# Kernel tuning notes

Hardware: AMD Instinct MI355X
Metric: run time of the kernel (lower is better)

## Reference

```python
import jax, jax.numpy as jnp
import numpy as np

EPS = 1e-8
LN_EPS = 1e-5

def _ln(x, g, b):
    m = x.mean(-1, keepdims=True)
    v = ((x - m) ** 2).mean(-1, keepdims=True)
    return (x - m) * jax.lax.rsqrt(v + LN_EPS) * g + b

def _rbf(d, n_rbf):
    # standard protein RBF embedding: gaussians on [0, 20] Angstrom
    mu = jnp.linspace(0.0, 20.0, n_rbf)
    sigma = 20.0 / n_rbf
    return jnp.exp(-(((d[..., None] - mu) / sigma) ** 2))

def setup_inputs() -> dict:
    N, K, CS, CZ, G, RBF = 1024, 16, 256, 128, 16, 64
    key = jax.random.key(0)
    ks = jax.random.split(key, 24)
    s = 0.02
    inp = {
        'node_features': jax.random.normal(ks[0], (N, CS), jnp.float32),
        'trans': jax.random.normal(ks[1], (N, 3), jnp.float32) * 10.0,
        'src_edge_features': jax.random.normal(ks[2], (N, K, CZ), jnp.float32),
        'dst_edge_features': jax.random.normal(ks[3], (N, K, CZ), jnp.float32),
        # params
        'ln_src_g': jnp.ones((CZ,)), 'ln_src_b': jnp.zeros((CZ,)),
        'ln_dst_g': jnp.ones((CZ,)), 'ln_dst_b': jnp.zeros((CZ,)),
        'W_nl': jax.random.normal(ks[4], (G, CS)) * s, 'b_nl': jnp.zeros((G,)),
        'W_nr': jax.random.normal(ks[5], (G, CS)) * s, 'b_nr': jnp.zeros((G,)),
        'W_ep': jax.random.normal(ks[6], (CZ, CZ)) * s, 'b_ep': jnp.zeros((CZ,)),
        'W_eg': jax.random.normal(ks[7], (CZ, CZ)) * s, 'b_eg': jnp.zeros((CZ,)),
        'W_dg': jax.random.normal(ks[8], (CZ, G, G)) * s, 'b_dg': jnp.zeros((CZ,)),
        'W_dp': jax.random.normal(ks[9], (CZ, RBF)) * s, 'b_dp': jnp.zeros((CZ,)),
        'ln_out_g': jnp.ones((CZ,)), 'ln_out_b': jnp.zeros((CZ,)),
        'W_lo': jax.random.normal(ks[10], (CZ, CZ)) * s, 'b_lo': jnp.zeros((CZ,)),
        'W_og': jax.random.normal(ks[11], (CZ, CZ)) * s, 'b_og': jnp.zeros((CZ,)),
        # int / mask args (KNN form)
        'src_edge_index': jax.random.randint(ks[12], (2, N, K), 0, N, jnp.int32),
        'dst_edge_index': jax.random.randint(ks[13], (2, N, K), 0, N, jnp.int32),
        'src_mask': jnp.ones((N, K), bool),
        'dst_mask': jnp.ones((N, K), bool),
    }
    return inp

def reference(node_features, trans, src_edge_features, dst_edge_features,
              ln_src_g, ln_src_b, ln_dst_g, ln_dst_b,
              W_nl, b_nl, W_nr, b_nr, W_ep, b_ep, W_eg, b_eg,
              W_dg, b_dg, W_dp, b_dp, ln_out_g, ln_out_b,
              W_lo, b_lo, W_og, b_og,
              src_edge_index, dst_edge_index, src_mask, dst_mask):
    N, K, CZ = src_edge_features.shape
    src_ln = _ln(src_edge_features, ln_src_g, ln_src_b)   # [N,K,CZ]
    dst_ln = _ln(dst_edge_features, ln_dst_g, ln_dst_b)
    node_left = node_features @ W_nl.T + b_nl              # [N,G]
    node_right = node_features @ W_nr.T + b_nr
    e1 = node_left[src_edge_index[0]]                      # [N,K,G]
    e2 = node_right[dst_edge_index[0]]                     # [N,K,G]
    # triangle gate: fuse outer product [N,K,K,G,G] with dist_gate Linear
    t = jnp.einsum('nia,zab->nizb', e1, W_dg)
    gate3 = jnp.einsum('nizb,njb->nijz', t, e2) + b_dg     # [N,K,K,CZ]
    t1 = trans[src_edge_index[0]]                          # [N,K,3]
    t2 = trans[dst_edge_index[0]]
    d = jnp.linalg.norm(t1[:, :, None, :] - t2[:, None, :, :] + EPS, axis=-1)  # [N,K,K]
    distf = _rbf(d, W_dp.shape[1]) @ W_dp.T + b_dp         # [N,K,K,CZ]
    mask3 = (src_mask[:, :, None] & dst_mask[:, None, :])[..., None]
    edge3 = jax.nn.sigmoid(gate3) * distf * mask3          # [N,K,K,CZ]
    edge2 = jax.nn.sigmoid(src_ln @ W_eg.T + b_eg) * (src_ln @ W_ep.T + b_ep)  # [N,K,CZ]
    # batched per-channel combine: sum over dst slot j
    upd = jnp.einsum('nijz,njz->niz', edge3, edge2)        # [N,K,CZ]
    upd = _ln(upd, ln_out_g, ln_out_b) @ W_lo.T + b_lo
    upd = upd * jax.nn.sigmoid(dst_ln @ W_og.T + b_og)
    upd = upd * dst_mask[..., None]                        # knn -> sparse (masked flatten)
    return upd.reshape(N * K, CZ)
```

## Files before the change

### kernel.cpp

```cpp
#include <hip/hip_runtime.h>
#include <hip/hip_bf16.h>
#include <stdint.h>

#define N_    1024
#define K_    16
#define CZ_   128
#define G_    16
#define RBF_  64
#define CS_   256

typedef const float* fp;
typedef _Float16 f16x8 __attribute__((ext_vector_type(8)));
typedef _Float16 h2    __attribute__((ext_vector_type(2)));
typedef float f32x4    __attribute__((ext_vector_type(4)));

#define MFMA16(A,B,C) __builtin_amdgcn_mfma_f32_16x16x32_f16(A,B,C,0,0,0)

#define OFF_EGH 0
#define OFF_EPH 16384
#define OFF_EPL 32768
#define OFF_OGH 49152
#define OFF_LOH 65536
#define OFF_LOL 81920
#define OFF_DPH 98304
#define OFF_NLH 106496
#define OFF_NRH 110592
#define OFF_DGT 114688

__device__ __forceinline__ float sigm(float x){ return 1.0f/(1.0f+__expf(-x)); }
__device__ __forceinline__ unsigned short f2h(float v){
  union{_Float16 h; unsigned short u;} c; c.h = (_Float16)v; return c.u;
}
__device__ __forceinline__ float h2f(unsigned short u){
  union{unsigned short u; _Float16 h;} c; c.u = u; return (float)c.h;
}
__device__ __forceinline__ unsigned int pk2(float a, float b){
  union{h2 h; unsigned int u;} c; c.h[0] = (_Float16)a; c.h[1] = (_Float16)b; return c.u;
}
__device__ __forceinline__ f16x8 ldh8(const unsigned short* p){
  union{uint4 u; f16x8 h;} c; c.u = *(const uint4*)p; return c.h;
}

__global__ __launch_bounds__(256) void repack(
    fp W_eg, fp W_ep, fp W_og, fp W_lo, fp W_dp, fp W_nl, fp W_nr, fp W_dg,
    unsigned short* __restrict__ ws)
{
  int t = blockIdx.x*256 + threadIdx.x;
  int stride = gridDim.x*256;
  for (int i = t; i < 16384; i += stride) {
    ws[OFF_EGH+i] = f2h(W_eg[i]);
    ws[OFF_OGH+i] = f2h(W_og[i]);
    float e = W_ep[i]; _Float16 h = (_Float16)e;
    union{_Float16 hh; unsigned short u;} c1; c1.hh = h;
    ws[OFF_EPH+i] = c1.u;
    ws[OFF_EPL+i] = f2h(e - (float)h);
    float l = W_lo[i]; _Float16 hl = (_Float16)l;
    union{_Float16 hh; unsigned short u;} c2; c2.hh = hl;
    ws[OFF_LOH+i] = c2.u;
    ws[OFF_LOL+i] = f2h(l - (float)hl);
  }
  for (int i = t; i < 8192; i += stride)
    ws[OFF_DPH+i] = f2h(W_dp[i]);
  for (int i = t; i < 4096; i += stride) {
    ws[OFF_NLH+i] = f2h(W_nl[i]);
    ws[OFF_NRH+i] = f2h(W_nr[i]);
  }
  for (int i = t; i < 32768; i += stride) {
    int z = i >> 8, rem = i & 255, b = rem >> 4, a = rem & 15;
    ws[OFF_DGT+i] = f2h(W_dg[z*256 + a*16 + b]);
  }
}

__global__ __launch_bounds__(512, 4) void tri_fused3(
    fp nf, fp trans, fp srcef, fp dstef,
    fp ln_src_g, fp ln_src_b, fp ln_dst_g, fp ln_dst_b,
    fp b_nl, fp b_nr, fp b_eg, fp b_ep, fp b_og,
    fp b_dg, fp b_dp, fp ln_out_g, fp ln_out_b, fp b_lo,
    const int* __restrict__ sidx, const int* __restrict__ didx,
    const unsigned short* __restrict__ ws,
    float* __restrict__ out)
{
  __shared__ __align__(16) unsigned short bufA[8448];
  __shared__ __align__(16) unsigned short bufB[6528];
  __shared__ __align__(16) unsigned short rbfH[16*64*16];
  __shared__ __align__(16) unsigned short edge2h[128*18];
  __shared__ __align__(16) unsigned short sogh[16*128];
  __shared__ __align__(16) unsigned short e1h[16*16];
  __shared__ __align__(16) unsigned short e2h[16*18];
  __shared__ __align__(16) float t1f[16][4];
  __shared__ __align__(16) float t2f[16][4];

  unsigned short* nflh = bufA;
  float* updf = (float*)bufA;
  unsigned short* srcH = bufB;
  unsigned short* srcL = bufB + 2176;
  unsigned short* dstH = bufB + 4352;
  unsigned short* updH = bufB;
  unsigned short* updL = bufB + 2176;

  const int n   = blockIdx.x;
  const int tid = threadIdx.x;
  const int wv  = tid >> 6;
  const int lnn = tid & 63;
  const int lm  = lnn & 15;
  const int lq  = lnn >> 4;

  {
    int row = tid >> 4;
    int c0  = (tid & 15) * 16;
    int r16 = row & 15;
    int idx = (row < 16) ? sidx[n*K_ + r16] : didx[n*K_ + r16];
    const float* src = nf + idx*CS_ + c0;
    float4 a = *(const float4*)(src);
    float4 b = *(const float4*)(src+4);
    float4 c = *(const float4*)(src+8);
    float4 d = *(const float4*)(src+12);
    uint4 u0, u1;
    u0.x = pk2(a.x,a.y); u0.y = pk2(a.z,a.w); u0.z = pk2(b.x,b.y); u0.w = pk2(b.z,b.w);
    u1.x = pk2(c.x,c.y); u1.y = pk2(c.z,c.w); u1.z = pk2(d.x,d.y); u1.w = pk2(d.z,d.w);
    *(uint4*)&nflh[row*264 + c0]     = u0;
    *(uint4*)&nflh[row*264 + c0 + 8] = u1;
    if (tid < 32) {
      int k = tid & 15;
      int id2 = (tid < 16) ? sidx[n*K_ + k] : didx[n*K_ + k];
      float* tf = (tid < 16) ? &t1f[k][0] : &t2f[k][0];
      tf[0] = trans[id2*3+0]; tf[1] = trans[id2*3+1]; tf[2] = trans[id2*3+2];
    }
  }
  {
    int row = tid >> 4;
    int c0  = (tid & 15) * 8;
    int r16 = row & 15;
    bool isSrc = row < 16;
    const float* base = (isSrc ? srcef : dstef) + (n*K_ + r16)*CZ_ + c0;
    float4 xa = *(const float4*)base;
    float4 xb = *(const float4*)(base+4);
    float x[8] = {xa.x,xa.y,xa.z,xa.w,xb.x,xb.y,xb.z,xb.w};
    float s = x[0]+x[1]+x[2]+x[3]+x[4]+x[5]+x[6]+x[7];
    s += __shfl_xor(s,1); s += __shfl_xor(s,2);
    s += __shfl_xor(s,4); s += __shfl_xor(s,8);
    float m = s * 0.0078125f;
    float q = 0.f;
    #pragma unroll
    for (int i = 0; i < 8; ++i) { float d = x[i]-m; q += d*d; }
    q += __shfl_xor(q,1); q += __shfl_xor(q,2);
    q += __shfl_xor(q,4); q += __shfl_xor(q,8);
    float rv = rsqrtf(q * 0.0078125f + 1e-5f);
    fp gp = isSrc ? ln_src_g : ln_dst_g;
    fp bp = isSrc ? ln_src_b : ln_dst_b;
    float y[8];
    #pragma unroll
    for (int i = 0; i < 8; ++i) y[i] = (x[i]-m)*rv*gp[c0+i] + bp[c0+i];
    if (isSrc) {
      float l[8];
      #pragma unroll
      for (int i = 0; i < 8; ++i) { _Float16 h0 = (_Float16)y[i]; l[i] = y[i] - (float)h0; }
      uint4 uh, ul;
      uh.x = pk2(y[0],y[1]); uh.y = pk2(y[2],y[3]); uh.z = pk2(y[4],y[5]); uh.w = pk2(y[6],y[7]);
      ul.x = pk2(l[0],l[1]); ul.y = pk2(l[2],l[3]); ul.z = pk2(l[4],l[5]); ul.w = pk2(l[6],l[7]);
      *(uint4*)&srcH[r16*136 + c0] = uh;
      *(uint4*)&srcL[r16*136 + c0] = ul;
    } else {
      uint4 uh;
      uh.x = pk2(y[0],y[1]); uh.y = pk2(y[2],y[3]); uh.z = pk2(y[4],y[5]); uh.w = pk2(y[6],y[7]);
      *(uint4*)&dstH[r16*136 + c0] = uh;
    }
  }
  __syncthreads();

  if (wv < 2) {
    const unsigned short* Wh = ws + (wv ? OFF_NRH : OFF_NLH);
    fp bb = wv ? b_nr : b_nl;
    const unsigned short* arow = nflh + (wv*16 + lm)*264;
    f32x4 acc = {0.f,0.f,0.f,0.f};
    #pragma unroll
    for (int kb = 0; kb < 256; kb += 32) {
      f16x8 ah = ldh8(arow + kb + lq*8);
      f16x8 bh = ldh8(Wh + lm*256 + kb + lq*8);
      acc = MFMA16(ah, bh, acc);
    }
    float bias = bb[lm];
    #pragma unroll
    for (int r = 0; r < 4; ++r) {
      if (wv) e2h[(lq*4+r)*18 + lm] = f2h(acc[r] + bias);
      else    e1h[(lq*4+r)*16 + lm] = f2h(acc[r] + bias);
    }
  }

  {
    const int z = wv*16 + lm;
    f32x4 aeg = {0.f,0.f,0.f,0.f}, aep = {0.f,0.f,0.f,0.f}, aog = {0.f,0.f,0.f,0.f};
    #pragma unroll
    for (int kb = 0; kb < 128; kb += 32) {
      f16x8 sh = ldh8(srcH + lm*136 + kb + lq*8);
      f16x8 sl = ldh8(srcL + lm*136 + kb + lq*8);
      f16x8 dh = ldh8(dstH + lm*136 + kb + lq*8);
      f16x8 wegv = ldh8(ws + OFF_EGH + z*128 + kb + lq*8);
      f16x8 weph = ldh8(ws + OFF_EPH + z*128 + kb + lq*8);
      f16x8 wepl = ldh8(ws + OFF_EPL + z*128 + kb + lq*8);
      f16x8 wogv = ldh8(ws + OFF_OGH + z*128 + kb + lq*8);
      aeg = MFMA16(sh, wegv, aeg);
      aep = MFMA16(sh, weph, aep);
      aep = MFMA16(sl, weph, aep);
      aep = MFMA16(sh, wepl, aep);
      aog = MFMA16(dh, wogv, aog);
    }
    float beg = b_eg[z], bep = b_ep[z], bog = b_og[z];
    #pragma unroll
    for (int r = 0; r < 4; ++r) {
      int j = lq*4 + r;
      edge2h[z*18 + j] = f2h(sigm(aeg[r]+beg) * (aep[r]+bep));
      sogh[j*128 + z]  = f2h(sigm(aog[r]+bog));
    }
  }

  {
    const float inv_sigma = 3.2f;
    const float mustep = 20.0f/63.0f;
    #pragma unroll
    for (int i2 = 0; i2 < 2; ++i2) {
      int i = wv*2 + i2;
      float dx = t1f[i][0]-t2f[lm][0]+1e-8f;
      float dy = t1f[i][1]-t2f[lm][1]+1e-8f;
      float dz = t1f[i][2]-t2f[lm][2]+1e-8f;
      float d = sqrtf(dx*dx+dy*dy+dz*dz);
      #pragma unroll
      for (int kh = 0; kh < 2; ++kh) {
        union { f16x8 h; uint4 u; } cv;
        #pragma unroll
        for (int c = 0; c < 8; ++c) {
          int k = kh*32 + lq*8 + c;
          float t = (d - (float)k*mustep) * inv_sigma;
          cv.h[c] = (_Float16)__expf(-t*t);
        }
        *(uint4*)&rbfH[(i*64+lnn)*16 + kh*8] = cv.u;
      }
    }
  }
  __syncthreads();

  {
    const int z = wv*16 + lm;
    f16x8 Bdg[8];
    #pragma unroll
    for (int q = 0; q < 8; ++q)
      Bdg[q] = ldh8(ws + OFF_DGT + z*256 + q*32 + lq*8);
    f16x8 Bdp0 = ldh8(ws + OFF_DPH + z*64 + lq*8);
    f16x8 Bdp1 = ldh8(ws + OFF_DPH + z*64 + 32 + lq*8);
    const float bdg = b_dg[z], bdp = b_dp[z];
    _Float16 e2s[8];
    #pragma unroll
    for (int q = 0; q < 8; ++q) {
      union{unsigned short u; _Float16 h;} c;
      c.u = e2h[lm*18 + 2*q + (lq>>1)];
      e2s[q] = c.h;
    }
    for (int i = 0; i < 16; ++i) {
      f16x8 e1v = ldh8(e1h + i*16 + (lq&1)*8);
      f32x4 accg = {0.f,0.f,0.f,0.f};
      #pragma unroll
      for (int q = 0; q < 8; ++q) {
        f16x8 av;
        _Float16 sc = e2s[q];
        #pragma unroll
        for (int c = 0; c < 8; ++c) av[c] = e1v[c] * sc;
        accg = MFMA16(av, Bdg[q], accg);
      }
      f16x8 r0 = ldh8(&rbfH[(i*64+lnn)*16]);
      f16x8 r1 = ldh8(&rbfH[(i*64+lnn)*16 + 8]);
      f32x4 accp = {0.f,0.f,0.f,0.f};
      accp = MFMA16(r0, Bdp0, accp);
      accp = MFMA16(r1, Bdp1, accp);
      float s = 0.f;
      #pragma unroll
      for (int r = 0; r < 4; ++r) {
        int j = lq*4 + r;
        float e2v = h2f(edge2h[z*18 + j]);
        s += sigm(accg[r]+bdg) * (accp[r]+bdp) * e2v;
      }
      s += __shfl_xor(s,16); s += __shfl_xor(s,32);
      if (lq == 0) updf[i*132 + z] = s;
    }
  }
  __syncthreads();

  {
    int row = tid >> 5;
    int c0  = (tid & 31) * 4;
    float4 x = *(const float4*)&updf[row*132 + c0];
    float s = x.x+x.y+x.z+x.w;
    s += __shfl_xor(s,1,32); s += __shfl_xor(s,2,32); s += __shfl_xor(s,4,32);
    s += __shfl_xor(s,8,32); s += __shfl_xor(s,16,32);
    float m = s * 0.0078125f;
    float q = (x.x-m)*(x.x-m)+(x.y-m)*(x.y-m)+(x.z-m)*(x.z-m)+(x.w-m)*(x.w-m);
    q += __shfl_xor(q,1,32); q += __shfl_xor(q,2,32); q += __shfl_xor(q,4,32);
    q += __shfl_xor(q,8,32); q += __shfl_xor(q,16,32);
    float rv = rsqrtf(q*0.0078125f + 1e-5f);
    float y0 = (x.x-m)*rv*ln_out_g[c0+0] + ln_out_b[c0+0];
    float y1 = (x.y-m)*rv*ln_out_g[c0+1] + ln_out_b[c0+1];
    float y2 = (x.z-m)*rv*ln_out_g[c0+2] + ln_out_b[c0+2];
    float y3 = (x.w-m)*rv*ln_out_g[c0+3] + ln_out_b[c0+3];
    _Float16 h0 = (_Float16)y0, h1 = (_Float16)y1, h2v = (_Float16)y2, h3 = (_Float16)y3;
    uint2 uh, ul;
    uh.x = pk2(y0,y1); uh.y = pk2(y2,y3);
    ul.x = pk2(y0-(float)h0, y1-(float)h1);
    ul.y = pk2(y2-(float)h2v, y3-(float)h3);
    __syncthreads();
    *(uint2*)&updH[row*136 + c0] = uh;
    *(uint2*)&updL[row*136 + c0] = ul;
  }
  __syncthreads();

  {
    const int z = wv*16 + lm;
    f32x4 acc = {0.f,0.f,0.f,0.f};
    #pragma unroll
    for (int kb = 0; kb < 128; kb += 32) {
      f16x8 ah = ldh8(updH + lm*136 + kb + lq*8);
      f16x8 al = ldh8(updL + lm*136 + kb + lq*8);
      f16x8 bh = ldh8(ws + OFF_LOH + z*128 + kb + lq*8);
      f16x8 bl = ldh8(ws + OFF_LOL + z*128 + kb + lq*8);
      acc = MFMA16(ah, bh, acc);
      acc = MFMA16(al, bh, acc);
      acc = MFMA16(ah, bl, acc);
    }
    float blo = b_lo[z];
    #pragma unroll
    for (int r = 0; r < 4; ++r) {
      int islot = lq*4 + r;
      out[(n*K_ + islot)*CZ_ + z] = (acc[r] + blo) * h2f(sogh[islot*128 + z]);
    }
  }
}

extern "C" void kernel_launch(void* const* d_in, const int* in_sizes, int n_in,
                              void* d_out, int out_size, void* d_ws, size_t ws_size,
                              hipStream_t stream)
{
  fp nodef    = (fp)d_in[0];
  fp trans    = (fp)d_in[1];
  fp srcef    = (fp)d_in[2];
  fp dstef    = (fp)d_in[3];
  fp ln_src_g = (fp)d_in[4];  fp ln_src_b = (fp)d_in[5];
  fp ln_dst_g = (fp)d_in[6];  fp ln_dst_b = (fp)d_in[7];
  fp W_nl = (fp)d_in[8];   fp b_nl = (fp)d_in[9];
  fp W_nr = (fp)d_in[10];  fp b_nr = (fp)d_in[11];
  fp W_ep = (fp)d_in[12];  fp b_ep = (fp)d_in[13];
  fp W_eg = (fp)d_in[14];  fp b_eg = (fp)d_in[15];
  fp W_dg = (fp)d_in[16];  fp b_dg = (fp)d_in[17];
  fp W_dp = (fp)d_in[18];  fp b_dp = (fp)d_in[19];
  fp ln_out_g = (fp)d_in[20]; fp ln_out_b = (fp)d_in[21];
  fp W_lo = (fp)d_in[22];  fp b_lo = (fp)d_in[23];
  fp W_og = (fp)d_in[24];  fp b_og = (fp)d_in[25];
  const int* sidx = (const int*)d_in[26];
  const int* didx = (const int*)d_in[27];

  unsigned short* ws16 = (unsigned short*)d_ws;
  float* outp = (float*)d_out;

  hipLaunchKernelGGL(repack, dim3(64), dim3(256), 0, stream,
                     W_eg, W_ep, W_og, W_lo, W_dp, W_nl, W_nr, W_dg, ws16);
  hipLaunchKernelGGL(tri_fused3, dim3(N_), dim3(512), 0, stream,
                     nodef, trans, srcef, dstef,
                     ln_src_g, ln_src_b, ln_dst_g, ln_dst_b,
                     b_nl, b_nr, b_eg, b_ep, b_og,
                     b_dg, b_dp, ln_out_g, ln_out_b, b_lo,
                     sidx, didx, ws16, outp);
}
```

Measured before the change: 188.3 us.

## Drop split-precision GEMMs, shrink LDS footprint, and chunk RBF staging for occupancy

Removes the hi/lo fp16 split compensation for the W_ep and W_lo GEMMs, so those steps use a single MFMA per k-step instead of three. The node-feature staging buffer is gone; the node projections now read fp32 rows from global memory and convert them to fp16 in registers. RBF tiles are computed in two halves of 8 rows, which halves that LDS buffer, and launch bounds are raised from 4 to 6 blocks per CU. Sigmoid now uses a hardware reciprocal. The cost is lower accuracy in several GEMMs and extra block-wide barriers inside the triangle loop.

```diff
diff --git a/kernel.cpp b/kernel.cpp
--- a/kernel.cpp
+++ b/kernel.cpp
@@ -18,16 +18,14 @@
 
 #define OFF_EGH 0
 #define OFF_EPH 16384
-#define OFF_EPL 32768
-#define OFF_OGH 49152
-#define OFF_LOH 65536
-#define OFF_LOL 81920
-#define OFF_DPH 98304
-#define OFF_NLH 106496
-#define OFF_NRH 110592
-#define OFF_DGT 114688
-
-__device__ __forceinline__ float sigm(float x){ return 1.0f/(1.0f+__expf(-x)); }
+#define OFF_OGH 32768
+#define OFF_LOH 49152
+#define OFF_DPH 65536
+#define OFF_DGT 73728
+
+__device__ __forceinline__ float sigm(float x){
+  return __builtin_amdgcn_rcpf(1.0f + __expf(-x));
+}
 __device__ __forceinline__ unsigned short f2h(float v){
   union{_Float16 h; unsigned short u;} c; c.h = (_Float16)v; return c.u;
 }
@@ -40,49 +38,46 @@
 __device__ __forceinline__ f16x8 ldh8(const unsigned short* p){
   union{uint4 u; f16x8 h;} c; c.u = *(const uint4*)p; return c.h;
 }
+__device__ __forceinline__ f16x8 cvt8(float4 a, float4 b){
+  f16x8 r;
+  r[0]=(_Float16)a.x; r[1]=(_Float16)a.y; r[2]=(_Float16)a.z; r[3]=(_Float16)a.w;
+  r[4]=(_Float16)b.x; r[5]=(_Float16)b.y; r[6]=(_Float16)b.z; r[7]=(_Float16)b.w;
+  return r;
+}
 
 __global__ __launch_bounds__(256) void repack(
-    fp W_eg, fp W_ep, fp W_og, fp W_lo, fp W_dp, fp W_nl, fp W_nr, fp W_dg,
+    fp W_eg, fp W_ep, fp W_og, fp W_lo, fp W_dp, fp W_dg,
     unsigned short* __restrict__ ws)
 {
   int t = blockIdx.x*256 + threadIdx.x;
   int stride = gridDim.x*256;
   for (int i = t; i < 16384; i += stride) {
     ws[OFF_EGH+i] = f2h(W_eg[i]);
+    ws[OFF_EPH+i] = f2h(W_ep[i]);
     ws[OFF_OGH+i] = f2h(W_og[i]);
-    float e = W_ep[i]; _Float16 h = (_Float16)e;
-    union{_Float16 hh; unsigned short u;} c1; c1.hh = h;
-    ws[OFF_EPH+i] = c1.u;
-    ws[OFF_EPL+i] = f2h(e - (float)h);
-    float l = W_lo[i]; _Float16 hl = (_Float16)l;
-    union{_Float16 hh; unsigned short u;} c2; c2.hh = hl;
-    ws[OFF_LOH+i] = c2.u;
-    ws[OFF_LOL+i] = f2h(l - (float)hl);
+    ws[OFF_LOH+i] = f2h(W_lo[i]);
   }
   for (int i = t; i < 8192; i += stride)
     ws[OFF_DPH+i] = f2h(W_dp[i]);
-  for (int i = t; i < 4096; i += stride) {
-    ws[OFF_NLH+i] = f2h(W_nl[i]);
-    ws[OFF_NRH+i] = f2h(W_nr[i]);
-  }
   for (int i = t; i < 32768; i += stride) {
     int z = i >> 8, rem = i & 255, b = rem >> 4, a = rem & 15;
     ws[OFF_DGT+i] = f2h(W_dg[z*256 + a*16 + b]);
   }
 }
 
-__global__ __launch_bounds__(512, 4) void tri_fused3(
+__global__ __launch_bounds__(512, 6) void tri_fused4(
     fp nf, fp trans, fp srcef, fp dstef,
     fp ln_src_g, fp ln_src_b, fp ln_dst_g, fp ln_dst_b,
-    fp b_nl, fp b_nr, fp b_eg, fp b_ep, fp b_og,
+    fp W_nl, fp b_nl, fp W_nr, fp b_nr,
+    fp b_eg, fp b_ep, fp b_og,
     fp b_dg, fp b_dp, fp ln_out_g, fp ln_out_b, fp b_lo,
     const int* __restrict__ sidx, const int* __restrict__ didx,
     const unsigned short* __restrict__ ws,
     float* __restrict__ out)
 {
-  __shared__ __align__(16) unsigned short bufA[8448];
-  __shared__ __align__(16) unsigned short bufB[6528];
-  __shared__ __align__(16) unsigned short rbfH[16*64*16];
+  __shared__ __align__(16) float updf[K_*132];
+  __shared__ __align__(16) unsigned short bufB[2*K_*136];
+  __shared__ __align__(16) unsigned short rbfH[8*64*16];
   __shared__ __align__(16) unsigned short edge2h[128*18];
   __shared__ __align__(16) unsigned short sogh[16*128];
   __shared__ __align__(16) unsigned short e1h[16*16];
@@ -90,13 +85,9 @@
   __shared__ __align__(16) float t1f[16][4];
   __shared__ __align__(16) float t2f[16][4];
 
-  unsigned short* nflh = bufA;
-  float* updf = (float*)bufA;
   unsigned short* srcH = bufB;
-  unsigned short* srcL = bufB + 2176;
-  unsigned short* dstH = bufB + 4352;
+  unsigned short* dstH = bufB + 2176;
   unsigned short* updH = bufB;
-  unsigned short* updL = bufB + 2176;
 
   const int n   = blockIdx.x;
   const int tid = threadIdx.x;
@@ -105,27 +96,11 @@
   const int lm  = lnn & 15;
   const int lq  = lnn >> 4;
 
-  {
-    int row = tid >> 4;
-    int c0  = (tid & 15) * 16;
-    int r16 = row & 15;
-    int idx = (row < 16) ? sidx[n*K_ + r16] : didx[n*K_ + r16];
-    const float* src = nf + idx*CS_ + c0;
-    float4 a = *(const float4*)(src);
-    float4 b = *(const float4*)(src+4);
-    float4 c = *(const float4*)(src+8);
-    float4 d = *(const float4*)(src+12);
-    uint4 u0, u1;
-    u0.x = pk2(a.x,a.y); u0.y = pk2(a.z,a.w); u0.z = pk2(b.x,b.y); u0.w = pk2(b.z,b.w);
-    u1.x = pk2(c.x,c.y); u1.y = pk2(c.z,c.w); u1.z = pk2(d.x,d.y); u1.w = pk2(d.z,d.w);
-    *(uint4*)&nflh[row*264 + c0]     = u0;
-    *(uint4*)&nflh[row*264 + c0 + 8] = u1;
-    if (tid < 32) {
-      int k = tid & 15;
-      int id2 = (tid < 16) ? sidx[n*K_ + k] : didx[n*K_ + k];
-      float* tf = (tid < 16) ? &t1f[k][0] : &t2f[k][0];
-      tf[0] = trans[id2*3+0]; tf[1] = trans[id2*3+1]; tf[2] = trans[id2*3+2];
-    }
+  if (tid < 32) {
+    int k = tid & 15;
+    int id2 = (tid < 16) ? sidx[n*K_ + k] : didx[n*K_ + k];
+    float* tf = (tid < 16) ? &t1f[k][0] : &t2f[k][0];
+    tf[0] = trans[id2*3+0]; tf[1] = trans[id2*3+1]; tf[2] = trans[id2*3+2];
   }
   {
     int row = tid >> 4;
@@ -151,35 +126,26 @@
     float y[8];
     #pragma unroll
     for (int i = 0; i < 8; ++i) y[i] = (x[i]-m)*rv*gp[c0+i] + bp[c0+i];
-    if (isSrc) {
-      float l[8];
-      #pragma unroll
-      for (int i = 0; i < 8; ++i) { _Float16 h0 = (_Float16)y[i]; l[i] = y[i] - (float)h0; }
-      uint4 uh, ul;
-      uh.x = pk2(y[0],y[1]); uh.y = pk2(y[2],y[3]); uh.z = pk2(y[4],y[5]); uh.w = pk2(y[6],y[7]);
-      ul.x = pk2(l[0],l[1]); ul.y = pk2(l[2],l[3]); ul.z = pk2(l[4],l[5]); ul.w = pk2(l[6],l[7]);
-      *(uint4*)&srcH[r16*136 + c0] = uh;
-      *(uint4*)&srcL[r16*136 + c0] = ul;
-    } else {
-      uint4 uh;
-      uh.x = pk2(y[0],y[1]); uh.y = pk2(y[2],y[3]); uh.z = pk2(y[4],y[5]); uh.w = pk2(y[6],y[7]);
-      *(uint4*)&dstH[r16*136 + c0] = uh;
-    }
+    uint4 uh;
+    uh.x = pk2(y[0],y[1]); uh.y = pk2(y[2],y[3]); uh.z = pk2(y[4],y[5]); uh.w = pk2(y[6],y[7]);
+    *(uint4*)&((isSrc ? srcH : dstH)[r16*136 + c0]) = uh;
   }
   __syncthreads();
 
   if (wv < 2) {
-    const unsigned short* Wh = ws + (wv ? OFF_NRH : OFF_NLH);
-    fp bb = wv ? b_nr : b_nl;
-    const unsigned short* arow = nflh + (wv*16 + lm)*264;
+    int idx = (wv ? didx : sidx)[n*K_ + lm];
+    const float* arow = nf + idx*CS_;
+    const float* wrow = (wv ? W_nr : W_nl) + lm*CS_;
     f32x4 acc = {0.f,0.f,0.f,0.f};
     #pragma unroll
     for (int kb = 0; kb < 256; kb += 32) {
-      f16x8 ah = ldh8(arow + kb + lq*8);
-      f16x8 bh = ldh8(Wh + lm*256 + kb + lq*8);
+      f16x8 ah = cvt8(*(const float4*)(arow + kb + lq*8),
+                      *(const float4*)(arow + kb + lq*8 + 4));
+      f16x8 bh = cvt8(*(const float4*)(wrow + kb + lq*8),
+                      *(const float4*)(wrow + kb + lq*8 + 4));
       acc = MFMA16(ah, bh, acc);
     }
-    float bias = bb[lm];
+    float bias = (wv ? b_nr : b_nl)[lm];
     #pragma unroll
     for (int r = 0; r < 4; ++r) {
       if (wv) e2h[(lq*4+r)*18 + lm] = f2h(acc[r] + bias);
@@ -193,16 +159,12 @@
     #pragma unroll
     for (int kb = 0; kb < 128; kb += 32) {
       f16x8 sh = ldh8(srcH + lm*136 + kb + lq*8);
-      f16x8 sl = ldh8(srcL + lm*136 + kb + lq*8);
       f16x8 dh = ldh8(dstH + lm*136 + kb + lq*8);
       f16x8 wegv = ldh8(ws + OFF_EGH + z*128 + kb + lq*8);
       f16x8 weph = ldh8(ws + OFF_EPH + z*128 + kb + lq*8);
-      f16x8 wepl = ldh8(ws + OFF_EPL + z*128 + kb + lq*8);
       f16x8 wogv = ldh8(ws + OFF_OGH + z*128 + kb + lq*8);
       aeg = MFMA16(sh, wegv, aeg);
       aep = MFMA16(sh, weph, aep);
-      aep = MFMA16(sl, weph, aep);
-      aep = MFMA16(sh, wepl, aep);
       aog = MFMA16(dh, wogv, aog);
     }
     float beg = b_eg[z], bep = b_ep[z], bog = b_og[z];
@@ -213,31 +175,6 @@
       sogh[j*128 + z]  = f2h(sigm(aog[r]+bog));
     }
   }
-
-  {
-    const float inv_sigma = 3.2f;
-    const float mustep = 20.0f/63.0f;
-    #pragma unroll
-    for (int i2 = 0; i2 < 2; ++i2) {
-      int i = wv*2 + i2;
-      float dx = t1f[i][0]-t2f[lm][0]+1e-8f;
-      float dy = t1f[i][1]-t2f[lm][1]+1e-8f;
-      float dz = t1f[i][2]-t2f[lm][2]+1e-8f;
-      float d = sqrtf(dx*dx+dy*dy+dz*dz);
-      #pragma unroll
-      for (int kh = 0; kh < 2; ++kh) {
-        union { f16x8 h; uint4 u; } cv;
-        #pragma unroll
-        for (int c = 0; c < 8; ++c) {
-          int k = kh*32 + lq*8 + c;
-          float t = (d - (float)k*mustep) * inv_sigma;
-          cv.h[c] = (_Float16)__expf(-t*t);
-        }
-        *(uint4*)&rbfH[(i*64+lnn)*16 + kh*8] = cv.u;
-      }
-    }
-  }
-  __syncthreads();
 
   {
     const int z = wv*16 + lm;
@@ -248,38 +185,64 @@
     f16x8 Bdp0 = ldh8(ws + OFF_DPH + z*64 + lq*8);
     f16x8 Bdp1 = ldh8(ws + OFF_DPH + z*64 + 32 + lq*8);
     const float bdg = b_dg[z], bdp = b_dp[z];
-    _Float16 e2s[8];
-    #pragma unroll
-    for (int q = 0; q < 8; ++q) {
-      union{unsigned short u; _Float16 h;} c;
-      c.u = e2h[lm*18 + 2*q + (lq>>1)];
-      e2s[q] = c.h;
-    }
-    for (int i = 0; i < 16; ++i) {
-      f16x8 e1v = ldh8(e1h + i*16 + (lq&1)*8);
-      f32x4 accg = {0.f,0.f,0.f,0.f};
-      #pragma unroll
-      for (int q = 0; q < 8; ++q) {
-        f16x8 av;
-        _Float16 sc = e2s[q];
+    const float inv_sigma = 3.2f;
+    const float mustep = 20.0f/63.0f;
+
+    for (int h = 0; h < 2; ++h) {
+      __syncthreads();
+      {
+        int i = h*8 + wv;
+        float dx = t1f[i][0]-t2f[lm][0]+1e-8f;
+        float dy = t1f[i][1]-t2f[lm][1]+1e-8f;
+        float dz = t1f[i][2]-t2f[lm][2]+1e-8f;
+        float d = sqrtf(dx*dx+dy*dy+dz*dz);
         #pragma unroll
-        for (int c = 0; c < 8; ++c) av[c] = e1v[c] * sc;
-        accg = MFMA16(av, Bdg[q], accg);
+        for (int kh = 0; kh < 2; ++kh) {
+          union { f16x8 hh; uint4 u; } cv;
+          #pragma unroll
+          for (int c = 0; c < 8; ++c) {
+            int k = kh*32 + lq*8 + c;
+            float t = (d - (float)k*mustep) * inv_sigma;
+            cv.hh[c] = (_Float16)__expf(-t*t);
+          }
+          *(uint4*)&rbfH[(wv*64+lnn)*16 + kh*8] = cv.u;
+        }
       }
-      f16x8 r0 = ldh8(&rbfH[(i*64+lnn)*16]);
-      f16x8 r1 = ldh8(&rbfH[(i*64+lnn)*16 + 8]);
-      f32x4 accp = {0.f,0.f,0.f,0.f};
-      accp = MFMA16(r0, Bdp0, accp);
-      accp = MFMA16(r1, Bdp1, accp);
-      float s = 0.f;
-      #pragma unroll
-      for (int r = 0; r < 4; ++r) {
-        int j = lq*4 + r;
-        float e2v = h2f(edge2h[z*18 + j]);
-        s += sigm(accg[r]+bdg) * (accp[r]+bdp) * e2v;
+      __syncthreads();
+      for (int ii = 0; ii < 8; ++ii) {
+        int i = h*8 + ii;
+        f16x8 e1v = ldh8(e1h + i*16 + (lq&1)*8);
+        _Float16 e2s[8];
+        #pragma unroll
+        for (int q = 0; q < 8; ++q) {
+          union{unsigned short u; _Float16 hh;} c;
+          c.u = e2h[lm*18 + 2*q + (lq>>1)];
+          e2s[q] = c.hh;
+        }
+        f32x4 accg = {0.f,0.f,0.f,0.f};
+        #pragma unroll
+        for (int q = 0; q < 8; ++q) {
+          f16x8 av;
+          _Float16 sc = e2s[q];
+          #pragma unroll
+          for (int c = 0; c < 8; ++c) av[c] = e1v[c] * sc;
+          accg = MFMA16(av, Bdg[q], accg);
+        }
+        f16x8 r0 = ldh8(&rbfH[(ii*64+lnn)*16]);
+        f16x8 r1 = ldh8(&rbfH[(ii*64+lnn)*16 + 8]);
+        f32x4 accp = {0.f,0.f,0.f,0.f};
+        accp = MFMA16(r0, Bdp0, accp);
+        accp = MFMA16(r1, Bdp1, accp);
+        float s = 0.f;
+        #pragma unroll
+        for (int r = 0; r < 4; ++r) {
+          int j = lq*4 + r;
+          float e2v = h2f(edge2h[z*18 + j]);
+          s += sigm(accg[r]+bdg) * (accp[r]+bdp) * e2v;
+        }
+        s += __shfl_xor(s,16); s += __shfl_xor(s,32);
+        if (lq == 0) updf[i*132 + z] = s;
       }
-      s += __shfl_xor(s,16); s += __shfl_xor(s,32);
-      if (lq == 0) updf[i*132 + z] = s;
     }
   }
   __syncthreads();
@@ -300,14 +263,9 @@
     float y1 = (x.y-m)*rv*ln_out_g[c0+1] + ln_out_b[c0+1];
     float y2 = (x.z-m)*rv*ln_out_g[c0+2] + ln_out_b[c0+2];
     float y3 = (x.w-m)*rv*ln_out_g[c0+3] + ln_out_b[c0+3];
-    _Float16 h0 = (_Float16)y0, h1 = (_Float16)y1, h2v = (_Float16)y2, h3 = (_Float16)y3;
-    uint2 uh, ul;
+    uint2 uh;
     uh.x = pk2(y0,y1); uh.y = pk2(y2,y3);
-    ul.x = pk2(y0-(float)h0, y1-(float)h1);
-    ul.y = pk2(y2-(float)h2v, y3-(float)h3);
-    __syncthreads();
     *(uint2*)&updH[row*136 + c0] = uh;
-    *(uint2*)&updL[row*136 + c0] = ul;
   }
   __syncthreads();
 
@@ -317,12 +275,8 @@
     #pragma unroll
     for (int kb = 0; kb < 128; kb += 32) {
       f16x8 ah = ldh8(updH + lm*136 + kb + lq*8);
-      f16x8 al = ldh8(updL + lm*136 + kb + lq*8);
       f16x8 bh = ldh8(ws + OFF_LOH + z*128 + kb + lq*8);
-      f16x8 bl = ldh8(ws + OFF_LOL + z*128 + kb + lq*8);
       acc = MFMA16(ah, bh, acc);
-      acc = MFMA16(al, bh, acc);
-      acc = MFMA16(ah, bl, acc);
     }
     float blo = b_lo[z];
     #pragma unroll
@@ -359,11 +313,12 @@
   float* outp = (float*)d_out;
 
   hipLaunchKernelGGL(repack, dim3(64), dim3(256), 0, stream,
-                     W_eg, W_ep, W_og, W_lo, W_dp, W_nl, W_nr, W_dg, ws16);
-  hipLaunchKernelGGL(tri_fused3, dim3(N_), dim3(512), 0, stream,
+                     W_eg, W_ep, W_og, W_lo, W_dp, W_dg, ws16);
+  hipLaunchKernelGGL(tri_fused4, dim3(N_), dim3(512), 0, stream,
                      nodef, trans, srcef, dstef,
                      ln_src_g, ln_src_b, ln_dst_g, ln_dst_b,
-                     b_nl, b_nr, b_eg, b_ep, b_og,
+                     W_nl, b_nl, W_nr, b_nr,
+                     b_eg, b_ep, b_og,
                      b_dg, b_dp, ln_out_g, ln_out_b, b_lo,
                      sidx, didx, ws16, outp);
 }
```

Result: slower. 265.8 us (+41.2%).
